# Optimization experiments

Hardware: AMD Instinct MI355X
Metric: run time of the kernel (lower is better)

The kernel has to match this reference:

```python
import jax, jax.numpy as jnp
import numpy as np

B, S, D, O, H, E, K = 4, 1024, 1024, 1024, 2048, 8, 2
EPS = 1e-5

def _layernorm(x, g, b):
    m = jnp.mean(x, axis=-1, keepdims=True)
    v = jnp.mean(jnp.square(x - m), axis=-1, keepdims=True)
    return (x - m) * jax.lax.rsqrt(v + EPS) * g + b

def setup_inputs() -> dict:
    key = jax.random.key(0)
    ks = jax.random.split(key, 8)
    def xavier(k, shape):
        fan_out, fan_in = shape[-2], shape[-1]
        bound = float(np.sqrt(6.0 / (fan_in + fan_out)))
        return jax.random.uniform(k, shape, jnp.float32, -bound, bound)
    return {
        "x": jax.random.normal(ks[0], (B, S, D), jnp.float32),
        "ln1_g": jnp.ones((D,), jnp.float32), "ln1_b": jnp.zeros((D,), jnp.float32),
        "router_w": xavier(ks[1], (E, D)), "router_b": jnp.zeros((E,), jnp.float32),
        "sh_w1": xavier(ks[2], (H, D)), "sh_b1": jnp.zeros((H,), jnp.float32),
        "sh_w2": xavier(ks[3], (O, H)), "sh_b2": jnp.zeros((O,), jnp.float32),
        "e_w1": xavier(ks[4], (E, H, D)), "e_b1": jnp.zeros((E, H), jnp.float32),
        "e_w2": xavier(ks[5], (E, O, H)), "e_b2": jnp.zeros((E, O), jnp.float32),
        "ln2_g": jnp.ones((O,), jnp.float32), "ln2_b": jnp.zeros((O,), jnp.float32),
    }

def reference(x, ln1_g, ln1_b, router_w, router_b, sh_w1, sh_b1, sh_w2, sh_b2,
              e_w1, e_b1, e_w2, e_b2, ln2_g, ln2_b):
    # eval mode: no router noise, no aux loss
    x_norm = _layernorm(x, ln1_g, ln1_b)               # [B,S,D]
    xf = x_norm.reshape(-1, D)                          # [T,D]
    logits = xf @ router_w.T + router_b                 # [T,E]
    probs = jax.nn.softmax(logits, axis=-1)
    tk_w, tk_i = jax.lax.top_k(probs, K)                # [T,K]
    tk_w = tk_w / jnp.sum(tk_w, axis=-1, keepdims=True)
    # shared expert (exact GELU, as torch nn.GELU default)
    shared = jax.nn.gelu(xf @ sh_w1.T + sh_b1, approximate=False) @ sh_w2.T + sh_b2  # [T,O]
    # all experts densely, combined sparsely by top-k weights
    hid = jax.nn.gelu(jnp.einsum('td,ehd->teh', xf, e_w1) + e_b1, approximate=False)  # [T,E,H]
    eout = jnp.einsum('teh,eoh->teo', hid, e_w2) + e_b2                                # [T,E,O]
    comb_w = jnp.sum(jax.nn.one_hot(tk_i, E, dtype=xf.dtype) * tk_w[..., None], axis=1)  # [T,E]
    out = shared * (1.0 / (E + 1)) + jnp.einsum('te,teo->to', comb_w, eout)           # [T,O]
    out = _layernorm(out.reshape(B, S, O), ln2_g, ln2_b)
    return out
```

## Files before the change

### kernel.cpp

```cpp
#include <hip/hip_runtime.h>
#include <math.h>
#include <stdint.h>

typedef unsigned short u16;
typedef unsigned int u32;

typedef __attribute__((ext_vector_type(8))) short bf16x8;
typedef __attribute__((ext_vector_type(4))) float f32x4;

#define ASYNC_COPY16(g, l)                                                         \
  __builtin_amdgcn_global_load_lds((__attribute__((address_space(1))) const void*)(g), \
                                   (__attribute__((address_space(3))) void*)(l), 16, 0, 0)

__device__ __forceinline__ float bf2f(u16 u) {
  union { u32 i; float f; } v; v.i = ((u32)u) << 16; return v.f;
}
__device__ __forceinline__ u16 f2bf(float f) {
  union { float f; u32 i; } v; v.f = f;
  u32 r = v.i + 0x7fffu + ((v.i >> 16) & 1u);
  return (u16)(r >> 16);
}
__device__ __forceinline__ float gelu_fast(float x) {
  float t = x * x;
  float z = 1.5957691f * x * (1.0f + 0.044715f * t);
  return x / (1.0f + __expf(-z));
}

__global__ __launch_bounds__(256) void cvt_all_k(
    const float* __restrict__ s0, const float* __restrict__ s1,
    const float* __restrict__ s2, const float* __restrict__ s3,
    u16* __restrict__ dst)
{
  const int64_t i0 = (int64_t)blockIdx.x * 2048 + (int64_t)threadIdx.x * 8;
  const float* src; int64_t rel;
  if (i0 < 2097152)       { src = s0; rel = i0; }
  else if (i0 < 4194304)  { src = s1; rel = i0 - 2097152; }
  else if (i0 < 20971520) { src = s2; rel = i0 - 4194304; }
  else                    { src = s3; rel = i0 - 20971520; }
  const float4 a = *(const float4*)(src + rel);
  const float4 b = *(const float4*)(src + rel + 4);
  union { u16 h[8]; uint4 v; } o;
  o.h[0] = f2bf(a.x); o.h[1] = f2bf(a.y); o.h[2] = f2bf(a.z); o.h[3] = f2bf(a.w);
  o.h[4] = f2bf(b.x); o.h[5] = f2bf(b.y); o.h[6] = f2bf(b.z); o.h[7] = f2bf(b.w);
  *(uint4*)(dst + i0) = o.v;
}

__global__ __launch_bounds__(256) void ln_router_k(
    const float* __restrict__ x, const float* __restrict__ g, const float* __restrict__ b,
    const float* __restrict__ rw, const float* __restrict__ rb,
    u16* __restrict__ xn, int* __restrict__ tk_idx, float* __restrict__ tk_w)
{
  const int t = blockIdx.x, tid = threadIdx.x;
  __shared__ float xs[1024];
  __shared__ float red[8];
  __shared__ float logits[8];
  const int wave = tid >> 6, lane = tid & 63;

  const float4 xv = *(const float4*)(x + (size_t)t * 1024 + 4 * tid);
  float v0 = xv.x, v1 = xv.y, v2 = xv.z, v3 = xv.w;
  float s = v0 + v1 + v2 + v3;
  float q = v0 * v0 + v1 * v1 + v2 * v2 + v3 * v3;
#pragma unroll
  for (int o = 32; o > 0; o >>= 1) { s += __shfl_down(s, o, 64); q += __shfl_down(q, o, 64); }
  if (lane == 0) { red[wave] = s; red[4 + wave] = q; }
  __syncthreads();
  if (tid == 0) {
    float S = red[0] + red[1] + red[2] + red[3];
    float Q = red[4] + red[5] + red[6] + red[7];
    float mean = S * (1.0f / 1024.0f);
    float var = Q * (1.0f / 1024.0f) - mean * mean;
    red[0] = mean; red[1] = rsqrtf(var + 1e-5f);
  }
  __syncthreads();
  const float mean = red[0], rstd = red[1];
  float vv[4] = {v0, v1, v2, v3};
  union { u16 h[4]; uint2 v; } pk;
#pragma unroll
  for (int j = 0; j < 4; ++j) {
    int d = 4 * tid + j;
    float y = (vv[j] - mean) * rstd * g[d] + b[d];
    xs[d] = y;
    pk.h[j] = f2bf(y);
  }
  *(uint2*)(xn + (size_t)t * 1024 + 4 * tid) = pk.v;
  __syncthreads();
#pragma unroll
  for (int pe = 0; pe < 2; ++pe) {
    int e = wave + 4 * pe;
    const float* wrow = rw + (size_t)e * 1024;
    float acc = 0.f;
#pragma unroll
    for (int j = 0; j < 16; ++j) {
      int d = lane + 64 * j;
      acc += xs[d] * wrow[d];
    }
#pragma unroll
    for (int o = 32; o > 0; o >>= 1) acc += __shfl_down(acc, o, 64);
    if (lane == 0) logits[e] = acc + rb[e];
  }
  __syncthreads();
  if (tid == 0) {
    int i0 = 0; float l0 = logits[0];
#pragma unroll
    for (int e = 1; e < 8; ++e) if (logits[e] > l0) { l0 = logits[e]; i0 = e; }
    int i1 = -1; float l1 = -3.4e38f;
#pragma unroll
    for (int e = 0; e < 8; ++e) { if (e == i0) continue; if (logits[e] > l1) { l1 = logits[e]; i1 = e; } }
    float w0 = 1.0f / (1.0f + expf(l1 - l0));
    float w1 = 1.0f - w0;
    tk_idx[2 * t] = i0; tk_idx[2 * t + 1] = i1;
    tk_w[2 * t] = w0; tk_w[2 * t + 1] = w1;
  }
}

__device__ __forceinline__ uint4 u4_add(uint4 a, uint4 b) {
  uint4 r; r.x = a.x + b.x; r.y = a.y + b.y; r.z = a.z + b.z; r.w = a.w + b.w; return r;
}
__device__ __forceinline__ uint4 u4_sub(uint4 a, uint4 b) {
  uint4 r; r.x = a.x - b.x; r.y = a.y - b.y; r.z = a.z - b.z; r.w = a.w - b.w; return r;
}

__global__ __launch_bounds__(256) void assign_k(
    const int* __restrict__ tk_idx, const float* __restrict__ tk_w,
    int* __restrict__ offs, int* __restrict__ slot_token,
    float* __restrict__ slot_w, int* __restrict__ slot_of)
{
  const int tid = threadIdx.x, lane = tid & 63, wave = tid >> 6;
  int eidx[32];
#pragma unroll
  for (int j = 0; j < 32; ++j) eidx[j] = tk_idx[tid * 32 + j];

  uint4 p = {0u, 0u, 0u, 0u};
#pragma unroll
  for (int j = 0; j < 32; ++j) {
    int e = eidx[j];
    unsigned inc = 1u << ((e & 1) * 16);
    int c = e >> 1;
    if (c == 0) p.x += inc; else if (c == 1) p.y += inc;
    else if (c == 2) p.z += inc; else p.w += inc;
  }
  const uint4 own = p;
#pragma unroll
  for (int o = 1; o < 64; o <<= 1) {
    uint4 t;
    t.x = (u32)__shfl_up((int)p.x, o, 64);
    t.y = (u32)__shfl_up((int)p.y, o, 64);
    t.z = (u32)__shfl_up((int)p.z, o, 64);
    t.w = (u32)__shfl_up((int)p.w, o, 64);
    if (lane >= o) p = u4_add(p, t);
  }
  __shared__ uint4 wtot[4];
  __shared__ int offs_s[9];
  if (lane == 63) wtot[wave] = p;
  __syncthreads();
  uint4 wbase = {0u, 0u, 0u, 0u};
  uint4 gtot = {0u, 0u, 0u, 0u};
#pragma unroll
  for (int w2 = 0; w2 < 4; ++w2) {
    uint4 t = wtot[w2];
    if (w2 < wave) wbase = u4_add(wbase, t);
    gtot = u4_add(gtot, t);
  }
  const uint4 excl = u4_sub(p, own);
  if (tid == 0) {
    int gtots[8] = { (int)(gtot.x & 0xffff), (int)(gtot.x >> 16),
                     (int)(gtot.y & 0xffff), (int)(gtot.y >> 16),
                     (int)(gtot.z & 0xffff), (int)(gtot.z >> 16),
                     (int)(gtot.w & 0xffff), (int)(gtot.w >> 16) };
    int a = 0;
#pragma unroll
    for (int e = 0; e < 8; ++e) { offs_s[e] = a; offs[e] = a; a += gtots[e]; }
    offs_s[8] = a; offs[8] = a;
  }
  __syncthreads();
  const uint4 pre = u4_add(wbase, excl);
  int base[8];
  base[0] = offs_s[0] + (int)(pre.x & 0xffff);
  base[1] = offs_s[1] + (int)(pre.x >> 16);
  base[2] = offs_s[2] + (int)(pre.y & 0xffff);
  base[3] = offs_s[3] + (int)(pre.y >> 16);
  base[4] = offs_s[4] + (int)(pre.z & 0xffff);
  base[5] = offs_s[5] + (int)(pre.z >> 16);
  base[6] = offs_s[6] + (int)(pre.w & 0xffff);
  base[7] = offs_s[7] + (int)(pre.w >> 16);
#pragma unroll
  for (int j = 0; j < 32; ++j) {
    int idx = tid * 32 + j;
    int e = eidx[j];
    int s = base[e]++;
    slot_token[s] = idx >> 1;
    slot_w[s] = tk_w[idx];
    slot_of[idx] = s;
  }
}

template <int N, int KD, int STAGE, int BK>
__global__ __launch_bounds__(512) void gemm2_k(
    const u16* __restrict__ Abase, const u16* __restrict__ Bsh,
    const u16* __restrict__ Bex, const float* __restrict__ bias_sh,
    const float* __restrict__ bias_ex,
    u16* __restrict__ outH,
    const int* __restrict__ offs, const int* __restrict__ slot_token,
    const float* __restrict__ slot_w, int nbase)
{
  constexpr int G    = BK / 8;
  constexpr int CH   = BK / 16;
  constexpr int RJ   = 512 / G;
  constexpr int TILE = 256 * BK;
  constexpr int KS   = BK / 32;

  const int tid = threadIdx.x;
  const int z = blockIdx.z;
  int off = 0, cnt = 4096, obase = 0;
  const u16* B = Bsh;
  const float* biasp = bias_sh;
  if (z > 0) {
    off = offs[z - 1]; cnt = offs[z] - off; obase = 4096 + off;
    B = Bex + (size_t)(z - 1) * N * KD;
    biasp = bias_ex + (size_t)(z - 1) * N;
  }
  const int m0 = blockIdx.y * 256;
  if (m0 >= cnt) return;
  const int n0 = nbase + blockIdx.x * 256;

  __shared__ u16 lds[2 * 2 * TILE];

  const int w = tid >> 6, l = tid & 63;

  const int rth = tid / G;
  const int pgt = tid % G;
  const int lg  = (BK == 64) ? (pgt ^ (rth & 7)) : (pgt ^ ((rth >> 1) & 3));

  const u16* gA[CH];
  const u16* gB[CH];
#pragma unroll
  for (int j = 0; j < CH; ++j) {
    int r = m0 + j * RJ + rth;
    if (r > cnt - 1) r = cnt - 1;
    size_t arow;
    if (STAGE == 1) arow = (z == 0) ? (size_t)r : (size_t)slot_token[off + r];
    else            arow = (z == 0) ? (size_t)r : (size_t)(4096 + off + r);
    gA[j] = Abase + arow * KD + lg * 8;
    gB[j] = B + (size_t)(n0 + j * RJ + rth) * KD + lg * 8;
  }

  const int wm = w >> 2, wn = w & 3;
  const int fr = l & 15, fq = l >> 4;
  const int swzm = (BK == 64) ? (fr & 7) : ((fr >> 1) & 3);
  const int rowA = (wm * 128 + fr) * BK;
  const int rowB = (wn * 64 + fr) * BK;

  f32x4 acc[8][4];
  const f32x4 zero = {0.f, 0.f, 0.f, 0.f};
#pragma unroll
  for (int mi = 0; mi < 8; ++mi)
#pragma unroll
    for (int ni = 0; ni < 4; ++ni) acc[mi][ni] = zero;

  const int NT = KD / BK;

#define STAGE_TILE(d)                                                       \
  { u16* dst = lds + (d) * 2 * TILE;                                        \
    _Pragma("unroll") for (int j = 0; j < CH; ++j) {                        \
      ASYNC_COPY16(gA[j], dst + j * 4096 + w * 512); gA[j] += BK; }         \
    _Pragma("unroll") for (int j = 0; j < CH; ++j) {                        \
      ASYNC_COPY16(gB[j], dst + TILE + j * 4096 + w * 512); gB[j] += BK; } }

  STAGE_TILE(0);

  for (int kb = 0; kb < NT; ++kb) {
    const int cur = kb & 1;
    __syncthreads();
    if (kb + 1 < NT) { STAGE_TILE(cur ^ 1); }

    const u16* sA = lds + cur * 2 * TILE;
    const u16* sB = sA + TILE;
#pragma unroll
    for (int ks = 0; ks < KS; ++ks) {
      const int sw = (((ks * 4 + fq) ^ swzm)) * 8;
      bf16x8 af[8], bv[4];
#pragma unroll
      for (int mi = 0; mi < 8; ++mi) af[mi] = *(const bf16x8*)(sA + rowA + mi * 16 * BK + sw);
#pragma unroll
      for (int ni = 0; ni < 4; ++ni) bv[ni] = *(const bf16x8*)(sB + rowB + ni * 16 * BK + sw);
#pragma unroll
      for (int mi = 0; mi < 8; ++mi)
#pragma unroll
        for (int ni = 0; ni < 4; ++ni)
          acc[mi][ni] = __builtin_amdgcn_mfma_f32_16x16x32_bf16(af[mi], bv[ni], acc[mi][ni], 0, 0, 0);
    }
  }

#pragma unroll
  for (int mi = 0; mi < 8; ++mi) {
    const int mlBase = m0 + wm * 128 + mi * 16 + fq * 4;
#pragma unroll
    for (int r = 0; r < 4; ++r) {
      const int ml = mlBase + r;
      if (ml >= cnt) continue;
      const size_t orow = (size_t)(obase + ml) * N;
      float rwgt = (STAGE == 2) ? ((z == 0) ? (1.0f / 9.0f) : slot_w[off + ml]) : 1.f;
#pragma unroll
      for (int ni = 0; ni < 4; ++ni) {
        const int col = n0 + wn * 64 + ni * 16 + fr;
        float v = acc[mi][ni][r] + biasp[col];
        if (STAGE == 1) v = gelu_fast(v);
        else            v = v * rwgt;
        outH[orow + col] = f2bf(v);
      }
    }
  }
#undef STAGE_TILE
}

__global__ __launch_bounds__(256) void combine_ln2_k(
    const u16* __restrict__ sh_out, const u16* __restrict__ eout,
    const int* __restrict__ slot_of,
    const float* __restrict__ g2, const float* __restrict__ b2,
    float* __restrict__ out)
{
  const int t = blockIdx.x, tid = threadIdx.x;
  const int wave = tid >> 6, lane = tid & 63;
  __shared__ float red[8];
  const size_t s0 = (size_t)slot_of[2 * t], s1 = (size_t)slot_of[2 * t + 1];
  union { uint2 v; u16 h[4]; } a, c0, c1;
  a.v  = *(const uint2*)(sh_out + (size_t)t * 1024 + 4 * tid);
  c0.v = *(const uint2*)(eout + s0 * 1024 + 4 * tid);
  c1.v = *(const uint2*)(eout + s1 * 1024 + 4 * tid);
  float vv[4];
#pragma unroll
  for (int j = 0; j < 4; ++j) vv[j] = bf2f(a.h[j]) + bf2f(c0.h[j]) + bf2f(c1.h[j]);
  float s = vv[0] + vv[1] + vv[2] + vv[3];
  float q = vv[0] * vv[0] + vv[1] * vv[1] + vv[2] * vv[2] + vv[3] * vv[3];
#pragma unroll
  for (int o = 32; o > 0; o >>= 1) { s += __shfl_down(s, o, 64); q += __shfl_down(q, o, 64); }
  if (lane == 0) { red[wave] = s; red[4 + wave] = q; }
  __syncthreads();
  if (tid == 0) {
    float S = red[0] + red[1] + red[2] + red[3];
    float Q = red[4] + red[5] + red[6] + red[7];
    float mean = S * (1.0f / 1024.0f);
    float var = Q * (1.0f / 1024.0f) - mean * mean;
    red[0] = mean; red[1] = rsqrtf(var + 1e-5f);
  }
  __syncthreads();
  const float mean = red[0], rstd = red[1];
#pragma unroll
  for (int j = 0; j < 4; ++j) {
    int d = 4 * tid + j;
    out[(size_t)t * 1024 + d] = (vv[j] - mean) * rstd * g2[d] + b2[d];
  }
}

extern "C" void kernel_launch(void* const* d_in, const int* in_sizes, int n_in,
                              void* d_out, int out_size, void* d_ws, size_t ws_size,
                              hipStream_t stream)
{
  const float* x     = (const float*)d_in[0];
  const float* ln1_g = (const float*)d_in[1];
  const float* ln1_b = (const float*)d_in[2];
  const float* rw    = (const float*)d_in[3];
  const float* rb    = (const float*)d_in[4];
  const float* sh_w1 = (const float*)d_in[5];
  const float* sh_b1 = (const float*)d_in[6];
  const float* sh_w2 = (const float*)d_in[7];
  const float* sh_b2 = (const float*)d_in[8];
  const float* e_w1  = (const float*)d_in[9];
  const float* e_b1  = (const float*)d_in[10];
  const float* e_w2  = (const float*)d_in[11];
  const float* e_b2  = (const float*)d_in[12];
  const float* ln2_g = (const float*)d_in[13];
  const float* ln2_b = (const float*)d_in[14];
  float* out = (float*)d_out;

  char* w = (char*)d_ws;
  u16*   x_norm = (u16*)(w + 0);
  u16*   hid    = (u16*)(w + (8u << 20));
  u16*   outb   = (u16*)(w + (56u << 20));
  u16*   w1b    = (u16*)(w + (104u << 20));
  u16*   w2b    = (u16*)(w + (108u << 20));
  u16*   ew1b   = (u16*)(w + (112u << 20));
  u16*   ew2b   = (u16*)(w + (144u << 20));
  char*  meta   = w + (176u << 20);
  int*   tk_idx     = (int*)(meta);
  float* tk_w       = (float*)(meta + (32u << 10));
  int*   slot_token = (int*)(meta + (64u << 10));
  float* slot_w     = (float*)(meta + (96u << 10));
  int*   slot_of    = (int*)(meta + (128u << 10));
  int*   offs       = (int*)(meta + (160u << 10));

  cvt_all_k<<<18432, 256, 0, stream>>>(sh_w1, sh_w2, e_w1, e_w2, w1b);

  ln_router_k<<<4096, 256, 0, stream>>>(x, ln1_g, ln1_b, rw, rb, x_norm, tk_idx, tk_w);
  assign_k<<<1, 256, 0, stream>>>(tk_idx, tk_w, offs, slot_token, slot_w, slot_of);

  gemm2_k<2048, 1024, 1, 64><<<dim3(4, 16, 9), 512, 0, stream>>>(
      x_norm, w1b, ew1b, sh_b1, e_b1, hid, offs, slot_token, nullptr, 0);
  gemm2_k<2048, 1024, 1, 32><<<dim3(4, 16, 9), 512, 0, stream>>>(
      x_norm, w1b, ew1b, sh_b1, e_b1, hid, offs, slot_token, nullptr, 1024);
  gemm2_k<1024, 2048, 2, 64><<<dim3(4, 16, 9), 512, 0, stream>>>(
      hid, w2b, ew2b, sh_b2, e_b2, outb, offs, slot_token, slot_w, 0);

  combine_ln2_k<<<4096, 256, 0, stream>>>(outb, outb + (size_t)4096 * 1024,
                                          slot_of, ln2_g, ln2_b, out);
}
```

Measured before the change: 492.0 us.

## Fuse weight conversion with LN/router, use atomic scatter, merge first GEMM launches

Weight fp32-to-bf16 conversion is folded into the LN/router kernel as extra grid-stride blocks, so both run in one launch. The single-block prefix-scan assignment kernel is replaced by atomic per-expert counters plus a 32-block atomic scatter. The two half-N first-layer GEMM launches are merged into one launch with a doubled grid.x. The aim is fewer launches, less serialization and more parallel work, at the cost of a memset, atomics and non-deterministic slot order within each expert.

```diff
diff --git a/kernel.cpp b/kernel.cpp
--- a/kernel.cpp
+++ b/kernel.cpp
@@ -26,31 +26,34 @@
   return x / (1.0f + __expf(-z));
 }
 
-__global__ __launch_bounds__(256) void cvt_all_k(
+__global__ __launch_bounds__(256) void pre_fused_k(
+    const float* __restrict__ x, const float* __restrict__ g, const float* __restrict__ b,
+    const float* __restrict__ rw, const float* __restrict__ rb,
+    u16* __restrict__ xn, int* __restrict__ tk_idx, float* __restrict__ tk_w,
+    int* __restrict__ cnt,
     const float* __restrict__ s0, const float* __restrict__ s1,
     const float* __restrict__ s2, const float* __restrict__ s3,
-    u16* __restrict__ dst)
-{
-  const int64_t i0 = (int64_t)blockIdx.x * 2048 + (int64_t)threadIdx.x * 8;
-  const float* src; int64_t rel;
-  if (i0 < 2097152)       { src = s0; rel = i0; }
-  else if (i0 < 4194304)  { src = s1; rel = i0 - 2097152; }
-  else if (i0 < 20971520) { src = s2; rel = i0 - 4194304; }
-  else                    { src = s3; rel = i0 - 20971520; }
-  const float4 a = *(const float4*)(src + rel);
-  const float4 b = *(const float4*)(src + rel + 4);
-  union { u16 h[8]; uint4 v; } o;
-  o.h[0] = f2bf(a.x); o.h[1] = f2bf(a.y); o.h[2] = f2bf(a.z); o.h[3] = f2bf(a.w);
-  o.h[4] = f2bf(b.x); o.h[5] = f2bf(b.y); o.h[6] = f2bf(b.z); o.h[7] = f2bf(b.w);
-  *(uint4*)(dst + i0) = o.v;
-}
-
-__global__ __launch_bounds__(256) void ln_router_k(
-    const float* __restrict__ x, const float* __restrict__ g, const float* __restrict__ b,
-    const float* __restrict__ rw, const float* __restrict__ rb,
-    u16* __restrict__ xn, int* __restrict__ tk_idx, float* __restrict__ tk_w)
-{
-  const int t = blockIdx.x, tid = threadIdx.x;
+    u16* __restrict__ wdst)
+{
+  const int bid = blockIdx.x, tid = threadIdx.x;
+  if (bid >= 4096) {
+    for (int c = bid - 4096; c < 18432; c += 4608) {
+      const int64_t i0 = (int64_t)c * 2048 + (int64_t)tid * 8;
+      const float* src; int64_t rel;
+      if (i0 < 2097152)       { src = s0; rel = i0; }
+      else if (i0 < 4194304)  { src = s1; rel = i0 - 2097152; }
+      else if (i0 < 20971520) { src = s2; rel = i0 - 4194304; }
+      else                    { src = s3; rel = i0 - 20971520; }
+      const float4 a = *(const float4*)(src + rel);
+      const float4 bb = *(const float4*)(src + rel + 4);
+      union { u16 h[8]; uint4 v; } o;
+      o.h[0] = f2bf(a.x);  o.h[1] = f2bf(a.y);  o.h[2] = f2bf(a.z);  o.h[3] = f2bf(a.w);
+      o.h[4] = f2bf(bb.x); o.h[5] = f2bf(bb.y); o.h[6] = f2bf(bb.z); o.h[7] = f2bf(bb.w);
+      *(uint4*)(wdst + i0) = o.v;
+    }
+    return;
+  }
+  const int t = bid;
   __shared__ float xs[1024];
   __shared__ float red[8];
   __shared__ float logits[8];
@@ -110,88 +113,29 @@
     float w1 = 1.0f - w0;
     tk_idx[2 * t] = i0; tk_idx[2 * t + 1] = i1;
     tk_w[2 * t] = w0; tk_w[2 * t + 1] = w1;
-  }
-}
-
-__device__ __forceinline__ uint4 u4_add(uint4 a, uint4 b) {
-  uint4 r; r.x = a.x + b.x; r.y = a.y + b.y; r.z = a.z + b.z; r.w = a.w + b.w; return r;
-}
-__device__ __forceinline__ uint4 u4_sub(uint4 a, uint4 b) {
-  uint4 r; r.x = a.x - b.x; r.y = a.y - b.y; r.z = a.z - b.z; r.w = a.w - b.w; return r;
-}
-
-__global__ __launch_bounds__(256) void assign_k(
+    atomicAdd(&cnt[i0], 1);
+    atomicAdd(&cnt[i1], 1);
+  }
+}
+
+__global__ __launch_bounds__(256) void scatter_k(
     const int* __restrict__ tk_idx, const float* __restrict__ tk_w,
+    const int* __restrict__ cnt, int* __restrict__ cursor,
     int* __restrict__ offs, int* __restrict__ slot_token,
     float* __restrict__ slot_w, int* __restrict__ slot_of)
 {
-  const int tid = threadIdx.x, lane = tid & 63, wave = tid >> 6;
-  int eidx[32];
-#pragma unroll
-  for (int j = 0; j < 32; ++j) eidx[j] = tk_idx[tid * 32 + j];
-
-  uint4 p = {0u, 0u, 0u, 0u};
-#pragma unroll
-  for (int j = 0; j < 32; ++j) {
-    int e = eidx[j];
-    unsigned inc = 1u << ((e & 1) * 16);
-    int c = e >> 1;
-    if (c == 0) p.x += inc; else if (c == 1) p.y += inc;
-    else if (c == 2) p.z += inc; else p.w += inc;
-  }
-  const uint4 own = p;
-#pragma unroll
-  for (int o = 1; o < 64; o <<= 1) {
-    uint4 t;
-    t.x = (u32)__shfl_up((int)p.x, o, 64);
-    t.y = (u32)__shfl_up((int)p.y, o, 64);
-    t.z = (u32)__shfl_up((int)p.z, o, 64);
-    t.w = (u32)__shfl_up((int)p.w, o, 64);
-    if (lane >= o) p = u4_add(p, t);
-  }
-  __shared__ uint4 wtot[4];
-  __shared__ int offs_s[9];
-  if (lane == 63) wtot[wave] = p;
-  __syncthreads();
-  uint4 wbase = {0u, 0u, 0u, 0u};
-  uint4 gtot = {0u, 0u, 0u, 0u};
-#pragma unroll
-  for (int w2 = 0; w2 < 4; ++w2) {
-    uint4 t = wtot[w2];
-    if (w2 < wave) wbase = u4_add(wbase, t);
-    gtot = u4_add(gtot, t);
-  }
-  const uint4 excl = u4_sub(p, own);
-  if (tid == 0) {
-    int gtots[8] = { (int)(gtot.x & 0xffff), (int)(gtot.x >> 16),
-                     (int)(gtot.y & 0xffff), (int)(gtot.y >> 16),
-                     (int)(gtot.z & 0xffff), (int)(gtot.z >> 16),
-                     (int)(gtot.w & 0xffff), (int)(gtot.w >> 16) };
-    int a = 0;
-#pragma unroll
-    for (int e = 0; e < 8; ++e) { offs_s[e] = a; offs[e] = a; a += gtots[e]; }
-    offs_s[8] = a; offs[8] = a;
-  }
-  __syncthreads();
-  const uint4 pre = u4_add(wbase, excl);
-  int base[8];
-  base[0] = offs_s[0] + (int)(pre.x & 0xffff);
-  base[1] = offs_s[1] + (int)(pre.x >> 16);
-  base[2] = offs_s[2] + (int)(pre.y & 0xffff);
-  base[3] = offs_s[3] + (int)(pre.y >> 16);
-  base[4] = offs_s[4] + (int)(pre.z & 0xffff);
-  base[5] = offs_s[5] + (int)(pre.z >> 16);
-  base[6] = offs_s[6] + (int)(pre.w & 0xffff);
-  base[7] = offs_s[7] + (int)(pre.w >> 16);
-#pragma unroll
-  for (int j = 0; j < 32; ++j) {
-    int idx = tid * 32 + j;
-    int e = eidx[j];
-    int s = base[e]++;
-    slot_token[s] = idx >> 1;
-    slot_w[s] = tk_w[idx];
-    slot_of[idx] = s;
-  }
+  int pre[8]; int a = 0;
+#pragma unroll
+  for (int e = 0; e < 8; ++e) { pre[e] = a; a += cnt[e]; }
+  const int idx = blockIdx.x * 256 + threadIdx.x;
+  const int e = tk_idx[idx];
+  const int pos = atomicAdd(&cursor[e], 1);
+  const int s = pre[e] + pos;
+  slot_token[s] = idx >> 1;
+  slot_w[s] = tk_w[idx];
+  slot_of[idx] = s;
+  if (blockIdx.x == 0 && threadIdx.x < 9)
+    offs[threadIdx.x] = (threadIdx.x == 8) ? a : pre[threadIdx.x];
 }
 
 template <int N, int KD, int STAGE, int BK>
@@ -388,16 +332,20 @@
   float* slot_w     = (float*)(meta + (96u << 10));
   int*   slot_of    = (int*)(meta + (128u << 10));
   int*   offs       = (int*)(meta + (160u << 10));
-
-  cvt_all_k<<<18432, 256, 0, stream>>>(sh_w1, sh_w2, e_w1, e_w2, w1b);
-
-  ln_router_k<<<4096, 256, 0, stream>>>(x, ln1_g, ln1_b, rw, rb, x_norm, tk_idx, tk_w);
-  assign_k<<<1, 256, 0, stream>>>(tk_idx, tk_w, offs, slot_token, slot_w, slot_of);
-
-  gemm2_k<2048, 1024, 1, 64><<<dim3(4, 16, 9), 512, 0, stream>>>(
+  int*   cnt        = (int*)(meta + (192u << 10));
+  int*   cursor     = cnt + 8;
+
+  hipMemsetAsync(cnt, 0, 16 * sizeof(int), stream);
+
+  pre_fused_k<<<8704, 256, 0, stream>>>(
+      x, ln1_g, ln1_b, rw, rb, x_norm, tk_idx, tk_w, cnt,
+      sh_w1, sh_w2, e_w1, e_w2, w1b);
+
+  scatter_k<<<32, 256, 0, stream>>>(tk_idx, tk_w, cnt, cursor,
+                                    offs, slot_token, slot_w, slot_of);
+
+  gemm2_k<2048, 1024, 1, 64><<<dim3(8, 16, 9), 512, 0, stream>>>(
       x_norm, w1b, ew1b, sh_b1, e_b1, hid, offs, slot_token, nullptr, 0);
-  gemm2_k<2048, 1024, 1, 32><<<dim3(4, 16, 9), 512, 0, stream>>>(
-      x_norm, w1b, ew1b, sh_b1, e_b1, hid, offs, slot_token, nullptr, 1024);
   gemm2_k<1024, 2048, 2, 64><<<dim3(4, 16, 9), 512, 0, stream>>>(
       hid, w2b, ew2b, sh_b2, e_b2, outb, offs, slot_token, slot_w, 0);
 
```

New measurement: 554.9 us. 1.13x slower.

## Fuse fp32-to-bf16 weight conversion into GEMM B-tile staging

Applied to the files above, without the earlier changes.

Removes the standalone kernel that converted all weights to bf16 each call. The GEMMs now load fp32 weight tiles into registers, convert them to bf16 and write them to LDS after the MFMA work, overlapping the global load with compute. This avoids a large extra read/write pass over the weights. The cost is doubled global bytes per B tile, re-read once per m-tile, plus extra register pressure and VALU conversion work. The first GEMM's two launches are also merged into a single grid.

```diff
diff --git a/kernel.cpp b/kernel.cpp
--- a/kernel.cpp
+++ b/kernel.cpp
@@ -24,25 +24,6 @@
   float t = x * x;
   float z = 1.5957691f * x * (1.0f + 0.044715f * t);
   return x / (1.0f + __expf(-z));
-}
-
-__global__ __launch_bounds__(256) void cvt_all_k(
-    const float* __restrict__ s0, const float* __restrict__ s1,
-    const float* __restrict__ s2, const float* __restrict__ s3,
-    u16* __restrict__ dst)
-{
-  const int64_t i0 = (int64_t)blockIdx.x * 2048 + (int64_t)threadIdx.x * 8;
-  const float* src; int64_t rel;
-  if (i0 < 2097152)       { src = s0; rel = i0; }
-  else if (i0 < 4194304)  { src = s1; rel = i0 - 2097152; }
-  else if (i0 < 20971520) { src = s2; rel = i0 - 4194304; }
-  else                    { src = s3; rel = i0 - 20971520; }
-  const float4 a = *(const float4*)(src + rel);
-  const float4 b = *(const float4*)(src + rel + 4);
-  union { u16 h[8]; uint4 v; } o;
-  o.h[0] = f2bf(a.x); o.h[1] = f2bf(a.y); o.h[2] = f2bf(a.z); o.h[3] = f2bf(a.w);
-  o.h[4] = f2bf(b.x); o.h[5] = f2bf(b.y); o.h[6] = f2bf(b.z); o.h[7] = f2bf(b.w);
-  *(uint4*)(dst + i0) = o.v;
 }
 
 __global__ __launch_bounds__(256) void ln_router_k(
@@ -194,25 +175,22 @@
   }
 }
 
-template <int N, int KD, int STAGE, int BK>
-__global__ __launch_bounds__(512) void gemm2_k(
-    const u16* __restrict__ Abase, const u16* __restrict__ Bsh,
-    const u16* __restrict__ Bex, const float* __restrict__ bias_sh,
-    const float* __restrict__ bias_ex,
+template <int N, int KD, int STAGE>
+__global__ __launch_bounds__(512) void gemm3_k(
+    const u16* __restrict__ Abase,
+    const float* __restrict__ Bsh, const float* __restrict__ Bex,
+    const float* __restrict__ bias_sh, const float* __restrict__ bias_ex,
     u16* __restrict__ outH,
     const int* __restrict__ offs, const int* __restrict__ slot_token,
-    const float* __restrict__ slot_w, int nbase)
-{
-  constexpr int G    = BK / 8;
-  constexpr int CH   = BK / 16;
-  constexpr int RJ   = 512 / G;
+    const float* __restrict__ slot_w)
+{
+  constexpr int BK   = 64;
   constexpr int TILE = 256 * BK;
-  constexpr int KS   = BK / 32;
 
   const int tid = threadIdx.x;
   const int z = blockIdx.z;
   int off = 0, cnt = 4096, obase = 0;
-  const u16* B = Bsh;
+  const float* B = Bsh;
   const float* biasp = bias_sh;
   if (z > 0) {
     off = offs[z - 1]; cnt = offs[z] - off; obase = 4096 + off;
@@ -221,32 +199,33 @@
   }
   const int m0 = blockIdx.y * 256;
   if (m0 >= cnt) return;
-  const int n0 = nbase + blockIdx.x * 256;
-
-  __shared__ u16 lds[2 * 2 * TILE];
-
-  const int w = tid >> 6, l = tid & 63;
-
-  const int rth = tid / G;
-  const int pgt = tid % G;
-  const int lg  = (BK == 64) ? (pgt ^ (rth & 7)) : (pgt ^ ((rth >> 1) & 3));
-
-  const u16* gA[CH];
-  const u16* gB[CH];
-#pragma unroll
-  for (int j = 0; j < CH; ++j) {
-    int r = m0 + j * RJ + rth;
+  const int n0 = blockIdx.x * 256;
+
+  __shared__ u16 lds[4 * TILE];
+
+  const int w = tid >> 6;
+
+  const int rth = tid >> 3;
+  const int pgt = tid & 7;
+  const int lg  = pgt ^ (rth & 7);
+
+  const u16*   gA[4];
+  const float* gB[4];
+#pragma unroll
+  for (int j = 0; j < 4; ++j) {
+    int r = m0 + j * 64 + rth;
     if (r > cnt - 1) r = cnt - 1;
     size_t arow;
     if (STAGE == 1) arow = (z == 0) ? (size_t)r : (size_t)slot_token[off + r];
     else            arow = (z == 0) ? (size_t)r : (size_t)(4096 + off + r);
     gA[j] = Abase + arow * KD + lg * 8;
-    gB[j] = B + (size_t)(n0 + j * RJ + rth) * KD + lg * 8;
-  }
-
+    gB[j] = B + (size_t)(n0 + j * 64 + rth) * KD + lg * 8;
+  }
+
+  const int l = tid & 63;
   const int wm = w >> 2, wn = w & 3;
   const int fr = l & 15, fq = l >> 4;
-  const int swzm = (BK == 64) ? (fr & 7) : ((fr >> 1) & 3);
+  const int swzm = fr & 7;
   const int rowA = (wm * 128 + fr) * BK;
   const int rowB = (wn * 64 + fr) * BK;
 
@@ -259,24 +238,42 @@
 
   const int NT = KD / BK;
 
-#define STAGE_TILE(d)                                                       \
+  float4 br[4][2];
+
+#define STAGE_A3(d)                                                         \
   { u16* dst = lds + (d) * 2 * TILE;                                        \
-    _Pragma("unroll") for (int j = 0; j < CH; ++j) {                        \
-      ASYNC_COPY16(gA[j], dst + j * 4096 + w * 512); gA[j] += BK; }         \
-    _Pragma("unroll") for (int j = 0; j < CH; ++j) {                        \
-      ASYNC_COPY16(gB[j], dst + TILE + j * 4096 + w * 512); gB[j] += BK; } }
-
-  STAGE_TILE(0);
+    _Pragma("unroll") for (int j = 0; j < 4; ++j) {                         \
+      ASYNC_COPY16(gA[j], dst + j * 4096 + w * 512); gA[j] += BK; } }
+#define LOADB3                                                              \
+  { _Pragma("unroll") for (int j = 0; j < 4; ++j) {                         \
+      br[j][0] = *(const float4*)(gB[j]);                                   \
+      br[j][1] = *(const float4*)(gB[j] + 4); gB[j] += BK; } }
+#define WRITEB3(d)                                                          \
+  { u16* dst = lds + (d) * 2 * TILE + TILE + tid * 8;                       \
+    _Pragma("unroll") for (int j = 0; j < 4; ++j) {                         \
+      union { u16 h[8]; uint4 v; } o;                                       \
+      o.h[0] = f2bf(br[j][0].x); o.h[1] = f2bf(br[j][0].y);                 \
+      o.h[2] = f2bf(br[j][0].z); o.h[3] = f2bf(br[j][0].w);                 \
+      o.h[4] = f2bf(br[j][1].x); o.h[5] = f2bf(br[j][1].y);                 \
+      o.h[6] = f2bf(br[j][1].z); o.h[7] = f2bf(br[j][1].w);                 \
+      *(uint4*)(dst + j * 4096) = o.v; } }
+
+  STAGE_A3(0);
+  LOADB3;
+  WRITEB3(0);
 
   for (int kb = 0; kb < NT; ++kb) {
     const int cur = kb & 1;
     __syncthreads();
-    if (kb + 1 < NT) { STAGE_TILE(cur ^ 1); }
+    if (kb + 1 < NT) {
+      STAGE_A3(cur ^ 1);
+      LOADB3;
+    }
 
     const u16* sA = lds + cur * 2 * TILE;
     const u16* sB = sA + TILE;
 #pragma unroll
-    for (int ks = 0; ks < KS; ++ks) {
+    for (int ks = 0; ks < 2; ++ks) {
       const int sw = (((ks * 4 + fq) ^ swzm)) * 8;
       bf16x8 af[8], bv[4];
 #pragma unroll
@@ -289,6 +286,8 @@
         for (int ni = 0; ni < 4; ++ni)
           acc[mi][ni] = __builtin_amdgcn_mfma_f32_16x16x32_bf16(af[mi], bv[ni], acc[mi][ni], 0, 0, 0);
     }
+
+    if (kb + 1 < NT) { WRITEB3(cur ^ 1); }
   }
 
 #pragma unroll
@@ -310,7 +309,9 @@
       }
     }
   }
-#undef STAGE_TILE
+#undef STAGE_A3
+#undef LOADB3
+#undef WRITEB3
 }
 
 __global__ __launch_bounds__(256) void combine_ln2_k(
@@ -377,10 +378,6 @@
   u16*   x_norm = (u16*)(w + 0);
   u16*   hid    = (u16*)(w + (8u << 20));
   u16*   outb   = (u16*)(w + (56u << 20));
-  u16*   w1b    = (u16*)(w + (104u << 20));
-  u16*   w2b    = (u16*)(w + (108u << 20));
-  u16*   ew1b   = (u16*)(w + (112u << 20));
-  u16*   ew2b   = (u16*)(w + (144u << 20));
   char*  meta   = w + (176u << 20);
   int*   tk_idx     = (int*)(meta);
   float* tk_w       = (float*)(meta + (32u << 10));
@@ -389,17 +386,13 @@
   int*   slot_of    = (int*)(meta + (128u << 10));
   int*   offs       = (int*)(meta + (160u << 10));
 
-  cvt_all_k<<<18432, 256, 0, stream>>>(sh_w1, sh_w2, e_w1, e_w2, w1b);
-
   ln_router_k<<<4096, 256, 0, stream>>>(x, ln1_g, ln1_b, rw, rb, x_norm, tk_idx, tk_w);
   assign_k<<<1, 256, 0, stream>>>(tk_idx, tk_w, offs, slot_token, slot_w, slot_of);
 
-  gemm2_k<2048, 1024, 1, 64><<<dim3(4, 16, 9), 512, 0, stream>>>(
-      x_norm, w1b, ew1b, sh_b1, e_b1, hid, offs, slot_token, nullptr, 0);
-  gemm2_k<2048, 1024, 1, 32><<<dim3(4, 16, 9), 512, 0, stream>>>(
-      x_norm, w1b, ew1b, sh_b1, e_b1, hid, offs, slot_token, nullptr, 1024);
-  gemm2_k<1024, 2048, 2, 64><<<dim3(4, 16, 9), 512, 0, stream>>>(
-      hid, w2b, ew2b, sh_b2, e_b2, outb, offs, slot_token, slot_w, 0);
+  gemm3_k<2048, 1024, 1><<<dim3(8, 16, 9), 512, 0, stream>>>(
+      x_norm, sh_w1, e_w1, sh_b1, e_b1, hid, offs, slot_token, nullptr);
+  gemm3_k<1024, 2048, 2><<<dim3(4, 16, 9), 512, 0, stream>>>(
+      hid, sh_w2, e_w2, sh_b2, e_b2, outb, offs, slot_token, slot_w);
 
   combine_ln2_k<<<4096, 256, 0, stream>>>(outb, outb + (size_t)4096 * 1024,
                                           slot_of, ln2_g, ln2_b, out);
```

Result: slower. 530.4 us (+7.8%).
